# Kernel tuning notes

Hardware: AMD Instinct MI355X
Metric: run time of the kernel (lower is better)

Reference implementation:

```python
import jax, jax.numpy as jnp
import numpy as np

BS, H, S, DK = 4, 16, 1024, 64  # bs, n_heads, seq_len(=q_len), head_dim


def setup_inputs() -> dict:
    key = jax.random.key(0)
    k1, k2, k3, k4 = jax.random.split(key, 4)
    return {
        "q": jax.random.normal(k1, (BS, H, S, DK), dtype=jnp.float32),
        "k": jax.random.normal(k2, (BS, H, DK, S), dtype=jnp.float32),
        "v": jax.random.normal(k3, (BS, H, S, DK), dtype=jnp.float32),
        "prev": jax.random.normal(k4, (BS, H, S, S), dtype=jnp.float32),
        "attn_mask": jnp.zeros((1, S, S), dtype=jnp.float32),  # additive float mask
        "key_padding_mask": jnp.zeros((BS, S), dtype=bool),     # True = masked key
        "scale": jnp.asarray(DK ** -0.5, dtype=jnp.float32),    # learnable (lsa=True)
    }


def reference(q, k, v, prev, attn_mask, key_padding_mask, scale):
    # attn_scores = q @ k * scale + prev + attn_mask (float branch)
    scores = jnp.einsum("bhqd,bhdk->bhqk", q, k) * scale
    scores = scores + prev + attn_mask[:, None, :, :]  # [1,S,S] -> broadcast over b,h
    # key_padding_mask: [bs, seq_len] -> masked_fill(-inf)
    scores = jnp.where(key_padding_mask[:, None, None, :], -jnp.inf, scores)
    attn = jax.nn.softmax(scores, axis=-1)  # dropout p=0.0 -> identity
    out = jnp.einsum("bhqk,bhkd->bhqd", attn, v)
    # res_attention=True -> (output, attn_weights, attn_scores)
    return out, attn, scores
```

## Files before the change

### kernel.cpp

```cpp
#include <hip/hip_runtime.h>
#include <math.h>

#define SEQ 1024
#define DKH 64
#define QBLK 16
#define NTILE 16
#define KSTR 68
#define ESTR 1032

typedef short s8v __attribute__((ext_vector_type(8)));
typedef short s4v __attribute__((ext_vector_type(4)));
typedef float f4v __attribute__((ext_vector_type(4)));

__device__ __forceinline__ short f2bf(float f) {
    unsigned u = __builtin_bit_cast(unsigned, f);
    return (short)((u + 0x8000u) >> 16);
}
__device__ __forceinline__ float bf2f(unsigned short h) {
    unsigned u = ((unsigned)h) << 16;
    return __builtin_bit_cast(float, u);
}
__device__ __forceinline__ s8v ld_frag(const unsigned short* p) {
    s4v a = *(const s4v*)(p);
    s4v b = *(const s4v*)(p + 4);
    s8v r;
    r[0]=a[0]; r[1]=a[1]; r[2]=a[2]; r[3]=a[3];
    r[4]=b[0]; r[5]=b[1]; r[6]=b[2]; r[7]=b[3];
    return r;
}

__global__ __launch_bounds__(256, 3)
void attn_fused(const float* __restrict__ q, const float* __restrict__ k,
                const float* __restrict__ v, const float* __restrict__ prev,
                const float* __restrict__ mask, const unsigned char* __restrict__ kpm,
                const float* __restrict__ scale_p,
                float* __restrict__ out, float* __restrict__ attn,
                float* __restrict__ scores)
{
    __shared__ unsigned short e_s[QBLK * ESTR];
    __shared__ unsigned short k_s[64 * KSTR];
    __shared__ unsigned short v_s[64 * KSTR];
    __shared__ float l_part[QBLK][4];
    __shared__ float inv_s[QBLK];

    const int t   = threadIdx.x;
    const int w   = t >> 6;
    const int l   = t & 63;
    const int g   = l >> 4;
    const int c16 = l & 15;
    const int sa  = t & 15, sg = t >> 4;

    const int wg  = blockIdx.x;
    const int swz = (wg & 7) * 512 + (wg >> 3);
    const int bh  = swz >> 6;
    const int rt  = swz & 63;
    const int b   = bh >> 4;

    const float scale = *scale_p;

    const float* qb = q    + ((size_t)bh * SEQ + rt * QBLK) * DKH;
    const float* kb = k    + (size_t)bh * DKH * SEQ;
    const float* vb = v    + (size_t)bh * SEQ * DKH;
    const float* pb = prev + ((size_t)bh * SEQ + rt * QBLK) * SEQ;
    const float* mb = mask + (size_t)(rt * QBLK) * SEQ;
    const unsigned char* kp = kpm + (size_t)b * SEQ;
    float* sb = scores + ((size_t)bh * SEQ + rt * QBLK) * SEQ;
    float* ab = attn   + ((size_t)bh * SEQ + rt * QBLK) * SEQ;
    float* ob = out    + ((size_t)bh * SEQ + rt * QBLK) * DKH;

    {
        const int row = t >> 4, c0 = (t & 15) * 4;
        f4v f = *(const f4v*)(qb + row * DKH + c0);
        s4v h; h[0]=f2bf(f[0]); h[1]=f2bf(f[1]); h[2]=f2bf(f[2]); h[3]=f2bf(f[3]);
        *(s4v*)&e_s[row * ESTR + c0] = h;
    }
    __syncthreads();
    const s8v aq0 = ld_frag(&e_s[c16 * ESTR + g * 8]);
    const s8v aq1 = ld_frag(&e_s[c16 * ESTR + 32 + g * 8]);

    f4v kreg[4], vreg[4];
    auto load_KV = [&](int ct) {
        const float* ksrc = kb + (size_t)(4 * sg) * SEQ + ct * 64 + 4 * sa;
        kreg[0] = *(const f4v*)(ksrc);
        kreg[1] = *(const f4v*)(ksrc + SEQ);
        kreg[2] = *(const f4v*)(ksrc + 2 * SEQ);
        kreg[3] = *(const f4v*)(ksrc + 3 * SEQ);
        const float* vsrc = vb + (size_t)(ct * 64 + 4 * sg) * DKH + 4 * sa;
        vreg[0] = *(const f4v*)(vsrc);
        vreg[1] = *(const f4v*)(vsrc + DKH);
        vreg[2] = *(const f4v*)(vsrc + 2 * DKH);
        vreg[3] = *(const f4v*)(vsrc + 3 * DKH);
    };
    float pr[4], mr[4];
    int kf;
    auto load_PM = [&](int ct) {
        const int col = ct * 64 + w * 16 + c16;
        #pragma unroll
        for (int r = 0; r < 4; ++r) {
            pr[r] = __builtin_nontemporal_load(pb + (size_t)(g * 4 + r) * SEQ + col);
            mr[r] = mb[(size_t)(g * 4 + r) * SEQ + col];
        }
        kf = kp[col];
    };

    float l_r[4] = {0.f, 0.f, 0.f, 0.f};
    f4v oacc = 0;

    load_KV(0);
    load_PM(0);

    for (int ct = 0; ct < NTILE; ++ct) {
        __syncthreads();
        #pragma unroll
        for (int j = 0; j < 4; ++j) {
            s4v hk; hk[0]=f2bf(kreg[0][j]); hk[1]=f2bf(kreg[1][j]); hk[2]=f2bf(kreg[2][j]); hk[3]=f2bf(kreg[3][j]);
            *(s4v*)&k_s[(4 * sa + j) * KSTR + 4 * sg] = hk;
            s4v hv; hv[0]=f2bf(vreg[0][j]); hv[1]=f2bf(vreg[1][j]); hv[2]=f2bf(vreg[2][j]); hv[3]=f2bf(vreg[3][j]);
            *(s4v*)&v_s[(4 * sa + j) * KSTR + 4 * sg] = hv;
        }
        __syncthreads();

        if (ct + 1 < NTILE) load_KV(ct + 1);

        f4v acc = 0;
        {
            const s8v bk0 = ld_frag(&k_s[(w * 16 + c16) * KSTR + g * 8]);
            const s8v bk1 = ld_frag(&k_s[(w * 16 + c16) * KSTR + 32 + g * 8]);
            acc = __builtin_amdgcn_mfma_f32_16x16x32_bf16(aq0, bk0, acc, 0, 0, 0);
            acc = __builtin_amdgcn_mfma_f32_16x16x32_bf16(aq1, bk1, acc, 0, 0, 0);
        }

        const int colb = ct * 64 + w * 16 + c16;
        #pragma unroll
        for (int r = 0; r < 4; ++r) {
            const int row = g * 4 + r;
            float x = fmaf(acc[r], scale, pr[r] + mr[r]);
            x = kf ? -INFINITY : x;
            __builtin_nontemporal_store(x, sb + (size_t)row * SEQ + colb);
            const float e = __expf(x);
            l_r[r] += e;
            e_s[row * ESTR + colb] = (unsigned short)f2bf(e);
        }
        if (ct + 1 < NTILE) load_PM(ct + 1);
        __syncthreads();

        {
            const s8v ae0 = ld_frag(&e_s[c16 * ESTR + ct * 64 + g * 8]);
            const s8v ae1 = ld_frag(&e_s[c16 * ESTR + ct * 64 + 32 + g * 8]);
            const s8v bv0 = ld_frag(&v_s[(w * 16 + c16) * KSTR + g * 8]);
            const s8v bv1 = ld_frag(&v_s[(w * 16 + c16) * KSTR + 32 + g * 8]);
            oacc = __builtin_amdgcn_mfma_f32_16x16x32_bf16(ae0, bv0, oacc, 0, 0, 0);
            oacc = __builtin_amdgcn_mfma_f32_16x16x32_bf16(ae1, bv1, oacc, 0, 0, 0);
        }
    }

    #pragma unroll
    for (int off = 1; off <= 8; off <<= 1) {
        #pragma unroll
        for (int r = 0; r < 4; ++r) l_r[r] += __shfl_xor(l_r[r], off, 64);
    }
    if (c16 == 0) {
        #pragma unroll
        for (int r = 0; r < 4; ++r) l_part[g * 4 + r][w] = l_r[r];
    }
    __syncthreads();
    if (t < QBLK)
        inv_s[t] = 1.0f / (l_part[t][0] + l_part[t][1] + l_part[t][2] + l_part[t][3]);
    __syncthreads();

    #pragma unroll
    for (int r = 0; r < 4; ++r)
        __builtin_nontemporal_store(oacc[r] * inv_s[g * 4 + r],
            ob + (size_t)(g * 4 + r) * DKH + w * 16 + c16);

    {
        const int row = t >> 4, i = t & 15;
        const float inv = inv_s[row];
        const unsigned short* erow = &e_s[row * ESTR];
        float* arow = ab + (size_t)row * SEQ;
        #pragma unroll
        for (int j = 0; j < 8; ++j) {
            const int c0 = (j * 16 + i) * 8;
            s8v h = ld_frag(erow + c0);
            f4v a0, a1;
            #pragma unroll
            for (int u = 0; u < 4; ++u) {
                a0[u] = bf2f((unsigned short)h[u]) * inv;
                a1[u] = bf2f((unsigned short)h[4 + u]) * inv;
            }
            __builtin_nontemporal_store(a0, (f4v*)(arow + c0));
            __builtin_nontemporal_store(a1, (f4v*)(arow + c0 + 4));
        }
    }
}

extern "C" void kernel_launch(void* const* d_in, const int* in_sizes, int n_in,
                              void* d_out, int out_size, void* d_ws, size_t ws_size,
                              hipStream_t stream) {
    const float* q    = (const float*)d_in[0];
    const float* k    = (const float*)d_in[1];
    const float* v    = (const float*)d_in[2];
    const float* prev = (const float*)d_in[3];
    const float* mask = (const float*)d_in[4];
    const unsigned char* kpm = (const unsigned char*)d_in[5];
    const float* scale = (const float*)d_in[6];

    float* out    = (float*)d_out;
    float* attn   = out  + (size_t)4 * 16 * SEQ * DKH;
    float* scores = attn + (size_t)4 * 16 * SEQ * SEQ;

    attn_fused<<<dim3(4096), dim3(256), 0, stream>>>(q, k, v, prev, mask, kpm, scale,
                                                     out, attn, scores);
}
```

Baseline: 306.7 us.

## Split into QK pass then PV pass with 128-column K/V groups

After: 304.3 us. About the same (-0.8%).

```diff
diff --git a/kernel.cpp b/kernel.cpp
--- a/kernel.cpp
+++ b/kernel.cpp
@@ -6,6 +6,7 @@
 #define QBLK 16
 #define NTILE 16
 #define KSTR 68
+#define VSTR 132
 #define ESTR 1032
 
 typedef short s8v __attribute__((ext_vector_type(8)));
@@ -19,6 +20,11 @@
 __device__ __forceinline__ float bf2f(unsigned short h) {
     unsigned u = ((unsigned)h) << 16;
     return __builtin_bit_cast(float, u);
+}
+__device__ __forceinline__ unsigned pk_bf16(float a, float b) {
+    unsigned ua = __builtin_bit_cast(unsigned, a);
+    unsigned ub = __builtin_bit_cast(unsigned, b);
+    return ((ub + 0x8000u) & 0xFFFF0000u) | ((ua + 0x8000u) >> 16);
 }
 __device__ __forceinline__ s8v ld_frag(const unsigned short* p) {
     s4v a = *(const s4v*)(p);
@@ -37,9 +43,8 @@
                 float* __restrict__ out, float* __restrict__ attn,
                 float* __restrict__ scores)
 {
+    __shared__ unsigned short kv_s[128 * KSTR];
     __shared__ unsigned short e_s[QBLK * ESTR];
-    __shared__ unsigned short k_s[64 * KSTR];
-    __shared__ unsigned short v_s[64 * KSTR];
     __shared__ float l_part[QBLK][4];
     __shared__ float inv_s[QBLK];
 
@@ -68,91 +73,113 @@
     float* ab = attn   + ((size_t)bh * SEQ + rt * QBLK) * SEQ;
     float* ob = out    + ((size_t)bh * SEQ + rt * QBLK) * DKH;
 
+    s8v aq0, aq1;
     {
-        const int row = t >> 4, c0 = (t & 15) * 4;
-        f4v f = *(const f4v*)(qb + row * DKH + c0);
-        s4v h; h[0]=f2bf(f[0]); h[1]=f2bf(f[1]); h[2]=f2bf(f[2]); h[3]=f2bf(f[3]);
-        *(s4v*)&e_s[row * ESTR + c0] = h;
-    }
-    __syncthreads();
-    const s8v aq0 = ld_frag(&e_s[c16 * ESTR + g * 8]);
-    const s8v aq1 = ld_frag(&e_s[c16 * ESTR + 32 + g * 8]);
-
-    f4v kreg[4], vreg[4];
-    auto load_KV = [&](int ct) {
-        const float* ksrc = kb + (size_t)(4 * sg) * SEQ + ct * 64 + 4 * sa;
-        kreg[0] = *(const f4v*)(ksrc);
-        kreg[1] = *(const f4v*)(ksrc + SEQ);
-        kreg[2] = *(const f4v*)(ksrc + 2 * SEQ);
-        kreg[3] = *(const f4v*)(ksrc + 3 * SEQ);
-        const float* vsrc = vb + (size_t)(ct * 64 + 4 * sg) * DKH + 4 * sa;
-        vreg[0] = *(const f4v*)(vsrc);
-        vreg[1] = *(const f4v*)(vsrc + DKH);
-        vreg[2] = *(const f4v*)(vsrc + 2 * DKH);
-        vreg[3] = *(const f4v*)(vsrc + 3 * DKH);
-    };
-    float pr[4], mr[4];
-    int kf;
-    auto load_PM = [&](int ct) {
+        const float* qr = qb + c16 * DKH + g * 8;
+        f4v q0 = *(const f4v*)(qr);
+        f4v q1 = *(const f4v*)(qr + 4);
+        f4v q2 = *(const f4v*)(qr + 32);
+        f4v q3 = *(const f4v*)(qr + 36);
+        uint4 r0, r1;
+        r0.x = pk_bf16(q0[0], q0[1]); r0.y = pk_bf16(q0[2], q0[3]);
+        r0.z = pk_bf16(q1[0], q1[1]); r0.w = pk_bf16(q1[2], q1[3]);
+        r1.x = pk_bf16(q2[0], q2[1]); r1.y = pk_bf16(q2[2], q2[3]);
+        r1.z = pk_bf16(q3[0], q3[1]); r1.w = pk_bf16(q3[2], q3[3]);
+        aq0 = __builtin_bit_cast(s8v, r0);
+        aq1 = __builtin_bit_cast(s8v, r1);
+    }
+
+    f4v streg[8];
+    auto load_Kgroup = [&](int grp) {
+        #pragma unroll
+        for (int sub = 0; sub < 2; ++sub) {
+            const float* src = kb + (size_t)(4 * sg) * SEQ + grp * 128 + sub * 64 + 4 * sa;
+            #pragma unroll
+            for (int i = 0; i < 4; ++i)
+                streg[sub * 4 + i] = *(const f4v*)(src + (size_t)i * SEQ);
+        }
+    };
+    auto load_Vgroup = [&](int grp) {
+        #pragma unroll
+        for (int sub = 0; sub < 2; ++sub) {
+            const float* src = vb + (size_t)(grp * 128 + sub * 64 + 4 * sg) * DKH + 4 * sa;
+            #pragma unroll
+            for (int i = 0; i < 4; ++i)
+                streg[sub * 4 + i] = *(const f4v*)(src + (size_t)i * DKH);
+        }
+    };
+
+    float prA[4], mrA[4], prB[4], mrB[4];
+    int kfA = 0, kfB = 0;
+    auto load_PM_A = [&](int ct) {
         const int col = ct * 64 + w * 16 + c16;
         #pragma unroll
         for (int r = 0; r < 4; ++r) {
-            pr[r] = __builtin_nontemporal_load(pb + (size_t)(g * 4 + r) * SEQ + col);
-            mr[r] = mb[(size_t)(g * 4 + r) * SEQ + col];
-        }
-        kf = kp[col];
+            prA[r] = __builtin_nontemporal_load(pb + (size_t)(g * 4 + r) * SEQ + col);
+            mrA[r] = mb[(size_t)(g * 4 + r) * SEQ + col];
+        }
+        kfA = kp[col];
+    };
+    auto load_PM_B = [&](int ct) {
+        const int col = ct * 64 + w * 16 + c16;
+        #pragma unroll
+        for (int r = 0; r < 4; ++r) {
+            prB[r] = __builtin_nontemporal_load(pb + (size_t)(g * 4 + r) * SEQ + col);
+            mrB[r] = mb[(size_t)(g * 4 + r) * SEQ + col];
+        }
+        kfB = kp[col];
     };
 
     float l_r[4] = {0.f, 0.f, 0.f, 0.f};
-    f4v oacc = 0;
-
-    load_KV(0);
-    load_PM(0);
-
-    for (int ct = 0; ct < NTILE; ++ct) {
-        __syncthreads();
-        #pragma unroll
-        for (int j = 0; j < 4; ++j) {
-            s4v hk; hk[0]=f2bf(kreg[0][j]); hk[1]=f2bf(kreg[1][j]); hk[2]=f2bf(kreg[2][j]); hk[3]=f2bf(kreg[3][j]);
-            *(s4v*)&k_s[(4 * sa + j) * KSTR + 4 * sg] = hk;
-            s4v hv; hv[0]=f2bf(vreg[0][j]); hv[1]=f2bf(vreg[1][j]); hv[2]=f2bf(vreg[2][j]); hv[3]=f2bf(vreg[3][j]);
-            *(s4v*)&v_s[(4 * sa + j) * KSTR + 4 * sg] = hv;
-        }
-        __syncthreads();
-
-        if (ct + 1 < NTILE) load_KV(ct + 1);
-
+
+    load_Kgroup(0);
+    load_PM_A(0);
+
+    auto qk_tile = [&](int ct, int sub, const float (&pr)[4], const float (&mr)[4], int kf) {
         f4v acc = 0;
         {
-            const s8v bk0 = ld_frag(&k_s[(w * 16 + c16) * KSTR + g * 8]);
-            const s8v bk1 = ld_frag(&k_s[(w * 16 + c16) * KSTR + 32 + g * 8]);
+            const s8v bk0 = ld_frag(&kv_s[(sub * 64 + w * 16 + c16) * KSTR + g * 8]);
             acc = __builtin_amdgcn_mfma_f32_16x16x32_bf16(aq0, bk0, acc, 0, 0, 0);
+            const s8v bk1 = ld_frag(&kv_s[(sub * 64 + w * 16 + c16) * KSTR + 32 + g * 8]);
             acc = __builtin_amdgcn_mfma_f32_16x16x32_bf16(aq1, bk1, acc, 0, 0, 0);
         }
-
-        const int colb = ct * 64 + w * 16 + c16;
+        const int col = ct * 64 + w * 16 + c16;
         #pragma unroll
         for (int r = 0; r < 4; ++r) {
             const int row = g * 4 + r;
             float x = fmaf(acc[r], scale, pr[r] + mr[r]);
             x = kf ? -INFINITY : x;
-            __builtin_nontemporal_store(x, sb + (size_t)row * SEQ + colb);
+            __builtin_nontemporal_store(x, sb + (size_t)row * SEQ + col);
             const float e = __expf(x);
             l_r[r] += e;
-            e_s[row * ESTR + colb] = (unsigned short)f2bf(e);
-        }
-        if (ct + 1 < NTILE) load_PM(ct + 1);
+            e_s[row * ESTR + col] = (unsigned short)f2bf(e);
+        }
+    };
+
+    #pragma unroll 1
+    for (int grp = 0; grp < 8; ++grp) {
+        if (grp) __syncthreads();
+        #pragma unroll
+        for (int sub = 0; sub < 2; ++sub) {
+            #pragma unroll
+            for (int j = 0; j < 4; ++j) {
+                s4v hk;
+                hk[0]=f2bf(streg[sub*4+0][j]); hk[1]=f2bf(streg[sub*4+1][j]);
+                hk[2]=f2bf(streg[sub*4+2][j]); hk[3]=f2bf(streg[sub*4+3][j]);
+                *(s4v*)&kv_s[(sub * 64 + 4 * sa + j) * KSTR + 4 * sg] = hk;
+            }
+        }
         __syncthreads();
-
-        {
-            const s8v ae0 = ld_frag(&e_s[c16 * ESTR + ct * 64 + g * 8]);
-            const s8v ae1 = ld_frag(&e_s[c16 * ESTR + ct * 64 + 32 + g * 8]);
-            const s8v bv0 = ld_frag(&v_s[(w * 16 + c16) * KSTR + g * 8]);
-            const s8v bv1 = ld_frag(&v_s[(w * 16 + c16) * KSTR + 32 + g * 8]);
-            oacc = __builtin_amdgcn_mfma_f32_16x16x32_bf16(ae0, bv0, oacc, 0, 0, 0);
-            oacc = __builtin_amdgcn_mfma_f32_16x16x32_bf16(ae1, bv1, oacc, 0, 0, 0);
-        }
-    }
+        if (grp + 1 < 8) load_Kgroup(grp + 1);
+
+        const int ct0 = grp * 2;
+        if (ct0 + 1 < NTILE) load_PM_B(ct0 + 1);
+        qk_tile(ct0, 0, prA, mrA, kfA);
+        if (ct0 + 2 < NTILE) load_PM_A(ct0 + 2);
+        qk_tile(ct0 + 1, 1, prB, mrB, kfB);
+    }
+
+    load_Vgroup(0);
 
     #pragma unroll
     for (int off = 1; off <= 8; off <<= 1) {
@@ -168,9 +195,42 @@
         inv_s[t] = 1.0f / (l_part[t][0] + l_part[t][1] + l_part[t][2] + l_part[t][3]);
     __syncthreads();
 
+    float inv_r[4];
+    #pragma unroll
+    for (int r = 0; r < 4; ++r) inv_r[r] = inv_s[g * 4 + r];
+
+    f4v oacc = 0;
+    #pragma unroll 1
+    for (int grp = 0; grp < 8; ++grp) {
+        if (grp) __syncthreads();
+        #pragma unroll
+        for (int sub = 0; sub < 2; ++sub) {
+            #pragma unroll
+            for (int j = 0; j < 4; ++j) {
+                s4v hv;
+                hv[0]=f2bf(streg[sub*4+0][j]); hv[1]=f2bf(streg[sub*4+1][j]);
+                hv[2]=f2bf(streg[sub*4+2][j]); hv[3]=f2bf(streg[sub*4+3][j]);
+                *(s4v*)&kv_s[(4 * sa + j) * VSTR + sub * 64 + 4 * sg] = hv;
+            }
+        }
+        __syncthreads();
+        if (grp + 1 < 8) load_Vgroup(grp + 1);
+
+        #pragma unroll
+        for (int sub = 0; sub < 2; ++sub) {
+            const int ct = grp * 2 + sub;
+            #pragma unroll
+            for (int ks = 0; ks < 2; ++ks) {
+                const s8v ae = ld_frag(&e_s[c16 * ESTR + ct * 64 + ks * 32 + g * 8]);
+                const s8v bv = ld_frag(&kv_s[(w * 16 + c16) * VSTR + sub * 64 + ks * 32 + g * 8]);
+                oacc = __builtin_amdgcn_mfma_f32_16x16x32_bf16(ae, bv, oacc, 0, 0, 0);
+            }
+        }
+    }
+
     #pragma unroll
     for (int r = 0; r < 4; ++r)
-        __builtin_nontemporal_store(oacc[r] * inv_s[g * 4 + r],
+        __builtin_nontemporal_store(oacc[r] * inv_r[r],
             ob + (size_t)(g * 4 + r) * DKH + w * 16 + c16);
 
     {
@@ -180,7 +240,7 @@
         float* arow = ab + (size_t)row * SEQ;
         #pragma unroll
         for (int j = 0; j < 8; ++j) {
-            const int c0 = (j * 16 + i) * 8;
+            const int c0 = j * 128 + i * 8;
             s8v h = ld_frag(erow + c0);
             f4v a0, a1;
             #pragma unroll
```
